# Kernel tuning notes

Hardware: AMD Instinct MI355X
Metric: run time of the kernel (lower is better)

## Reference

```python
import jax, jax.numpy as jnp
import numpy as np

N = 50000        # nodes
E = 150000       # edges
D_IN = 42        # node_input_dim
D_H = 42         # node_hidden_dim
E_IN = 10        # edge_input_dim
E_H = 128        # edge_hidden_dim
STEPS = 6        # num_step_message_passing


def _linear_params(key, fin, fout):
    k1, k2 = jax.random.split(key)
    bound = 1.0 / np.sqrt(fin)
    W = jax.random.uniform(k1, (fin, fout), minval=-bound, maxval=bound, dtype=jnp.float32)
    b = jax.random.uniform(k2, (fout,), minval=-bound, maxval=bound, dtype=jnp.float32)
    return W, b


def setup_inputs() -> dict:
    key = jax.random.key(0)
    ks = jax.random.split(key, 9)
    n_feat = jax.random.normal(ks[0], (N, D_IN), dtype=jnp.float32)
    e_feat = jax.random.normal(ks[1], (E, E_IN), dtype=jnp.float32)
    src = jax.random.randint(ks[2], (E,), 0, N, dtype=jnp.int32)
    dst = jax.random.randint(ks[3], (E,), 0, N, dtype=jnp.int32)
    lin0_w, lin0_b = _linear_params(ks[4], D_IN, D_H)
    en1_w, en1_b = _linear_params(ks[5], E_IN, E_H)
    en2_w, en2_b = _linear_params(ks[6], E_H, D_H * D_H)
    msg_w, msg_b = _linear_params(ks[7], 2 * D_H, D_H)
    conv_bias = jnp.zeros((D_H,), dtype=jnp.float32)  # NNConv bias
    return dict(n_feat=n_feat, e_feat=e_feat, src=src, dst=dst,
                lin0_w=lin0_w, lin0_b=lin0_b,
                en1_w=en1_w, en1_b=en1_b, en2_w=en2_w, en2_b=en2_b,
                conv_bias=conv_bias, msg_w=msg_w, msg_b=msg_b)


def reference(n_feat, e_feat, src, dst, lin0_w, lin0_b, en1_w, en1_b,
              en2_w, en2_b, conv_bias, msg_w, msg_b):
    init = n_feat
    out = jax.nn.relu(n_feat @ lin0_w + lin0_b)          # [N, D_H]
    # edge network: per-edge weight matrix (constant across the 6 steps)
    h_e = jax.nn.relu(e_feat @ en1_w + en1_b)            # [E, E_H]
    W_e = (h_e @ en2_w + en2_b).reshape(E, D_H, D_H)     # [E, D_H, D_H]
    for _ in range(STEPS):
        # NNConv: gather src feats, per-edge matmul, scatter-sum to dst,
        # identity residual (in==out feats) + bias
        msg = jnp.einsum('ei,eio->eo', out[src], W_e)    # [E, D_H]
        aggr = jax.ops.segment_sum(msg, dst, num_segments=N)
        m = jax.nn.relu(aggr + out + conv_bias)          # relu(conv(...))
        out = jnp.concatenate([m, out], axis=1) @ msg_w + msg_b
    return out + init
```

## Files before the change

### kernel.cpp

```cpp
#include <hip/hip_runtime.h>

typedef unsigned short u16;
typedef unsigned int u32;

#define NN 50000
#define NE 150000
#define D 42
#define EH 128
#define DD 1764
#define STEPS 6
#define MS 48
#define SCAN_NB 196

typedef __attribute__((ext_vector_type(8))) short bf8;
typedef __attribute__((ext_vector_type(4))) float f4;

static __device__ __forceinline__ float bf2f(u16 v) {
  return __uint_as_float(((u32)v) << 16);
}
static __device__ __forceinline__ u16 f2bf(float f) {
  u32 x = __float_as_uint(f);
  return (u16)((x + 0x7fffu + ((x >> 16) & 1u)) >> 16);
}

__global__ void k_detect(const u32* __restrict__ words, int* __restrict__ flag) {
  __shared__ int cnt;
  if (threadIdx.x == 0) cnt = 0;
  __syncthreads();
  int bad = 0;
  for (int i = threadIdx.x; i < 4096; i += 256) {
    u32 w = words[i];
    float v = __uint_as_float((w & 0xffffu) << 16);
    float a = fabsf(v);
    if (!(a < 16.0f)) bad++;
  }
  if (bad) atomicAdd(&cnt, bad);
  __syncthreads();
  if (threadIdx.x == 0) flag[0] = (cnt < 100) ? 1 : 0;
}

__global__ void k_cvt(const void* __restrict__ src, float* __restrict__ dst,
                      int count, const int* __restrict__ flag) {
  int i = blockIdx.x * blockDim.x + threadIdx.x;
  if (i >= count) return;
  if (flag[0]) dst[i] = bf2f(((const u16*)src)[i]);
  else         dst[i] = ((const float*)src)[i];
}

__global__ void k_hist(const int* __restrict__ dstI, int* __restrict__ cnt) {
  int e = blockIdx.x * blockDim.x + threadIdx.x;
  if (e < NE) atomicAdd(&cnt[dstI[e]], 1);
}

__global__ void k_scanA(const int* __restrict__ cnt, int* __restrict__ loc,
                        int* __restrict__ part) {
  __shared__ int wsum[4];
  int tid = threadIdx.x, wid = tid >> 6, lane = tid & 63;
  int i = blockIdx.x * 256 + tid;
  int v = (i < NN) ? cnt[i] : 0;
#pragma unroll
  for (int d = 1; d < 64; d <<= 1) {
    int t = __shfl_up(v, d, 64);
    if (lane >= d) v += t;
  }
  if (lane == 63) wsum[wid] = v;
  __syncthreads();
  if (tid == 0) {
    int s = 0;
#pragma unroll
    for (int w2 = 0; w2 < 4; ++w2) { int t = wsum[w2]; wsum[w2] = s; s += t; }
    part[blockIdx.x] = s;
  }
  __syncthreads();
  v += wsum[wid];
  if (i < NN) loc[i] = v;
}

__global__ void k_scanB(int* __restrict__ part) {
  __shared__ int wsum[4];
  int tid = threadIdx.x, wid = tid >> 6, lane = tid & 63;
  int v = (tid < SCAN_NB) ? part[tid] : 0;
  int orig = v;
#pragma unroll
  for (int d = 1; d < 64; d <<= 1) {
    int t = __shfl_up(v, d, 64);
    if (lane >= d) v += t;
  }
  if (lane == 63) wsum[wid] = v;
  __syncthreads();
  if (tid == 0) {
    int s = 0;
#pragma unroll
    for (int w2 = 0; w2 < 4; ++w2) { int t = wsum[w2]; wsum[w2] = s; s += t; }
  }
  __syncthreads();
  v += wsum[wid];
  if (tid < SCAN_NB) part[tid] = v - orig;
}

__global__ void k_scanC(const int* __restrict__ loc, const int* __restrict__ part,
                        int* __restrict__ rs) {
  int i = blockIdx.x * 256 + threadIdx.x;
  if (i == 0) rs[0] = 0;
  if (i < NN) rs[i + 1] = loc[i] + part[blockIdx.x];
}

__global__ void k_rank(const int* __restrict__ dstI, const int* __restrict__ srcI,
                       int* __restrict__ cursor, int* __restrict__ rank,
                       int* __restrict__ srcS) {
  int e = blockIdx.x * blockDim.x + threadIdx.x;
  if (e >= NE) return;
  int p = atomicAdd(&cursor[dstI[e]], 1);
  rank[e] = p;
  srcS[p] = srcI[e];
}

__global__ void k_lin0(const float* __restrict__ nf, const float* __restrict__ w,
                       const float* __restrict__ b, float* __restrict__ outp) {
  int gid = blockIdx.x * blockDim.x + threadIdx.x;
  int n = gid >> 6, lane = gid & 63;
  if (n >= NN) return;
  float xv = (lane < D) ? nf[(size_t)n * D + lane] : 0.f;
  if (lane < D) {
    float acc = b[lane];
    for (int i = 0; i < D; ++i)
      acc += __shfl(xv, i, 64) * w[i * D + lane];
    outp[(size_t)n * D + lane] = fmaxf(acc, 0.f);
  }
}

__global__ void k_en1(const float* __restrict__ ef, const float* __restrict__ w,
                      const float* __restrict__ b, const int* __restrict__ rank,
                      u16* __restrict__ h) {
  int gid = blockIdx.x * blockDim.x + threadIdx.x;
  int e = gid >> 7, k = gid & 127;
  if (e >= NE) return;
  float acc = b[k];
#pragma unroll
  for (int i = 0; i < 10; ++i)
    acc += ef[(size_t)e * 10 + i] * w[i * EH + k];
  h[(size_t)rank[e] * EH + k] = f2bf(fmaxf(acc, 0.f));
}

__global__ void k_packA(const float* __restrict__ w2, u16* __restrict__ Ap) {
  int idx = blockIdx.x * 256 + threadIdx.x;
  if (idx >= D * 4 * 3 * 64 * 8) return;
  int j = idx & 7;
  int t = idx >> 3;
  int l = t & 63; t >>= 6;
  int f = t % 3;  t /= 3;
  int s = t & 3;
  int i = t >> 2;
  int k = s * 32 + ((l >> 4) << 3) + j;
  int o = f * 16 + (l & 15);
  float v = (o < D) ? w2[(size_t)k * DD + i * D + o] : 0.f;
  Ap[idx] = f2bf(v);
}

__global__ void k_packB2(const float* __restrict__ e2b, u16* __restrict__ b2p) {
  int idx = blockIdx.x * 256 + threadIdx.x;
  if (idx >= 2 * 3 * 64 * 8) return;
  int j = idx & 7;
  int t = idx >> 3;
  int l = t & 63; t >>= 6;
  int f = t % 3;
  int s = t / 3;
  int k = s * 32 + ((l >> 4) << 3) + j;
  int o = f * 16 + (l & 15);
  float v = (k < D && o < D) ? e2b[k * D + o] : 0.f;
  b2p[idx] = f2bf(v);
}

__launch_bounds__(256, 3)
__global__ void k_edge_mfma(const float* __restrict__ outp, const u16* __restrict__ hbf,
                            const u16* __restrict__ Ap, const u16* __restrict__ b2p,
                            const int* __restrict__ srcS, float* __restrict__ msg) {
  __shared__ __align__(16) char smem[10752 + 26624];
  float* xT = (float*)smem;
  char*  hls = smem + 10752;
  char*  xbf = smem + 10752 + 16384;
  float* red = (float*)(smem + 10752);

  int tid = threadIdx.x;
  long et = (long)blockIdx.x * 64;
  int ne = (int)(NE - et); if (ne > 64) ne = 64;

  for (int c = tid; c < 1024; c += 256) {
    int row = c >> 4;
    int off = (c & 15) << 4;
    uint4 v = {0, 0, 0, 0};
    if (row < ne) v = *(const uint4*)(hbf + (et + row) * EH + (off >> 1));
    *(uint4*)(hls + row * 256 + (off ^ ((row & 7) << 4))) = v;
  }
  {
    int r = tid >> 2, j = tid & 3;
    const float* xr = (r < ne) ? (outp + (size_t)srcS[et + r] * D) : nullptr;
    for (int i = j; i < D; i += 4) {
      float v = xr ? xr[i] : 0.f;
      xT[i * 64 + r] = v;
      int bo = (r * 128 + i * 2) ^ ((r & 7) << 4);
      *(u16*)(xbf + bo) = f2bf(v);
    }
    for (int i = D + j; i < 64; i += 4) {
      int bo = (r * 128 + i * 2) ^ ((r & 7) << 4);
      *(u16*)(xbf + bo) = 0;
    }
  }
  __syncthreads();

  int w = tid >> 6;
  int l = tid & 63;
  int e16 = l & 15;
  int kg = l >> 4;

  bf8 hf[4];
  {
    int kb = (w * 32 + kg * 8) * 2;
    int sw = (e16 & 7) << 4;
#pragma unroll
    for (int g = 0; g < 4; ++g)
      hf[g] = *(const bf8*)(hls + (g * 16 + e16) * 256 + (kb ^ sw));
  }

  f4 macc[4][3];
#pragma unroll
  for (int g = 0; g < 4; ++g)
#pragma unroll
    for (int f = 0; f < 3; ++f)
      macc[g][f] = (f4){0.f, 0.f, 0.f, 0.f};

  const u16* apw = Ap + (size_t)w * 1536 + (size_t)l * 8;

#define COMPUTE(ii, AA)                                                         \
  {                                                                             \
    _Pragma("unroll")                                                           \
    for (int g = 0; g < 4; ++g) {                                               \
      float xs = xT[(ii) * 64 + g * 16 + e16];                                  \
      f4 zz = {0.f, 0.f, 0.f, 0.f};                                             \
      f4 q0 = __builtin_amdgcn_mfma_f32_16x16x32_bf16(AA[0], hf[g], zz, 0, 0, 0); \
      f4 q1 = __builtin_amdgcn_mfma_f32_16x16x32_bf16(AA[1], hf[g], zz, 0, 0, 0); \
      f4 q2 = __builtin_amdgcn_mfma_f32_16x16x32_bf16(AA[2], hf[g], zz, 0, 0, 0); \
      macc[g][0] += xs * q0;                                                    \
      macc[g][1] += xs * q1;                                                    \
      macc[g][2] += xs * q2;                                                    \
    }                                                                           \
  }

  bf8 A0[3], A1[3];
#pragma unroll
  for (int f = 0; f < 3; ++f) A0[f] = *(const bf8*)(apw + f * 512);
#pragma unroll 1
  for (int i = 0; i < D; i += 2) {
    const u16* pn = apw + (size_t)(i + 1) * 6144;
#pragma unroll
    for (int f = 0; f < 3; ++f) A1[f] = *(const bf8*)(pn + f * 512);
    COMPUTE(i, A0);
    if (i + 2 < D) {
      const u16* pn2 = apw + (size_t)(i + 2) * 6144;
#pragma unroll
      for (int f = 0; f < 3; ++f) A0[f] = *(const bf8*)(pn2 + f * 512);
    }
    COMPUTE(i + 1, A1);
  }

  if (w < 2) {
    const u16* bpw = b2p + (size_t)w * 1536 + (size_t)l * 8;
    bf8 B0 = *(const bf8*)(bpw);
    bf8 B1 = *(const bf8*)(bpw + 512);
    bf8 B2 = *(const bf8*)(bpw + 1024);
    int kb = (w * 32 + kg * 8) * 2;
    int sw = (e16 & 7) << 4;
#pragma unroll
    for (int g = 0; g < 4; ++g) {
      bf8 bx = *(const bf8*)(xbf + (g * 16 + e16) * 128 + (kb ^ sw));
      macc[g][0] = __builtin_amdgcn_mfma_f32_16x16x32_bf16(B0, bx, macc[g][0], 0, 0, 0);
      macc[g][1] = __builtin_amdgcn_mfma_f32_16x16x32_bf16(B1, bx, macc[g][1], 0, 0, 0);
      macc[g][2] = __builtin_amdgcn_mfma_f32_16x16x32_bf16(B2, bx, macc[g][2], 0, 0, 0);
    }
  }

  __syncthreads();
  if (w < 2) {
#pragma unroll
    for (int g = 0; g < 4; ++g)
#pragma unroll
      for (int f = 0; f < 3; ++f)
        *(f4*)&red[((size_t)w * 64 + g * 16 + e16) * 52 + f * 16 + kg * 4] = macc[g][f];
  }
  __syncthreads();
  if (w >= 2) {
#pragma unroll
    for (int g = 0; g < 4; ++g)
#pragma unroll
      for (int f = 0; f < 3; ++f) {
        float* rp = &red[((size_t)(w - 2) * 64 + g * 16 + e16) * 52 + f * 16 + kg * 4];
        f4 v = *(f4*)rp;
        v += macc[g][f];
        *(f4*)rp = v;
      }
  }
  __syncthreads();
  {
    int e = tid >> 2, c = tid & 3;
    if (e < ne) {
      float* mrow = msg + (size_t)(et + e) * MS;
#pragma unroll
      for (int u = 0; u < 3; ++u) {
        int o0 = c * 12 + u * 4;
        f4 v0 = *(f4*)&red[(size_t)e * 52 + o0];
        f4 v1 = *(f4*)&red[((size_t)(64 + e)) * 52 + o0];
        f4 s = v0 + v1;
        *(f4*)(mrow + o0) = s;
      }
    }
  }
#undef COMPUTE
}

__global__ void k_node_update(const float* __restrict__ msg, const int* __restrict__ rs,
                              const float* __restrict__ outp,
                              const float* __restrict__ cb, const float* __restrict__ mw,
                              const float* __restrict__ mb, float* __restrict__ newout,
                              const float* __restrict__ nf, void* __restrict__ fout,
                              int last, const int* __restrict__ flag) {
  int gid = blockIdx.x * blockDim.x + threadIdx.x;
  int n = gid >> 6, lane = gid & 63;
  if (n >= NN) return;
  float ov = (lane < D) ? outp[(size_t)n * D + lane] : 0.f;
  float av = 0.f;
  int r0 = rs[n], r1 = rs[n + 1];
  if (lane < D && r0 < r1) {
    float a0 = 0.f, a1 = 0.f, a2 = 0.f, a3 = 0.f;
    for (int r = r0; r < r1; r += 4) {
      int i1 = (r + 1 < r1) ? r + 1 : r;
      int i2 = (r + 2 < r1) ? r + 2 : r;
      int i3 = (r + 3 < r1) ? r + 3 : r;
      float v0 = msg[(size_t)r  * MS + lane];
      float v1 = msg[(size_t)i1 * MS + lane];
      float v2 = msg[(size_t)i2 * MS + lane];
      float v3 = msg[(size_t)i3 * MS + lane];
      a0 += v0;
      a1 += (r + 1 < r1) ? v1 : 0.f;
      a2 += (r + 2 < r1) ? v2 : 0.f;
      a3 += (r + 3 < r1) ? v3 : 0.f;
    }
    av = (a0 + a1) + (a2 + a3);
  }
  float mv = 0.f;
  if (lane < D) mv = fmaxf(av + ov + cb[lane], 0.f);
  if (lane < D) {
    float acc = mb[lane];
    for (int i = 0; i < D; ++i)
      acc += __shfl(mv, i, 64) * mw[i * D + lane];
    for (int i = 0; i < D; ++i)
      acc += __shfl(ov, i, 64) * mw[(D + i) * D + lane];
    size_t idx = (size_t)n * D + lane;
    if (last) {
      float res = acc + nf[idx];
      if (flag[0]) ((u16*)fout)[idx] = f2bf(res);
      else         ((float*)fout)[idx] = res;
    } else {
      newout[idx] = acc;
    }
  }
}

extern "C" void kernel_launch(void* const* d_in, const int* in_sizes, int n_in,
                              void* d_out, int out_size, void* d_ws, size_t ws_size,
                              hipStream_t stream) {
  (void)in_sizes; (void)n_in; (void)out_size; (void)ws_size;
  const void* nf   = d_in[0];
  const void* ef   = d_in[1];
  const int*  srcI = (const int*)d_in[2];
  const int*  dstI = (const int*)d_in[3];
  const void* l0w = d_in[4];  const void* l0b = d_in[5];
  const void* e1w = d_in[6];  const void* e1b = d_in[7];
  const void* e2w = d_in[8];  const void* e2b = d_in[9];
  const void* cbI = d_in[10]; const void* mwI = d_in[11]; const void* mbI = d_in[12];

  char* ws = (char*)d_ws;
  size_t off = 0;
  auto alloc = [&](size_t bytes) -> void* {
    void* p = ws + off;
    off = (off + bytes + 255) & ~(size_t)255;
    return p;
  };

  int*   flag  = (int*)alloc(4);
  float* c_nf  = (float*)alloc((size_t)NN * D * 4);
  float* c_ef  = (float*)alloc((size_t)NE * 10 * 4);
  float* c_l0w = (float*)alloc(D * D * 4);
  float* c_l0b = (float*)alloc(D * 4);
  float* c_e1w = (float*)alloc(10 * EH * 4);
  float* c_e1b = (float*)alloc(EH * 4);
  float* c_e2w = (float*)alloc((size_t)EH * DD * 4);
  float* c_e2b = (float*)alloc(DD * 4);
  float* c_cb  = (float*)alloc(D * 4);
  float* c_mw  = (float*)alloc(2 * D * D * 4);
  float* c_mb  = (float*)alloc(D * 4);
  float* out_a = (float*)alloc((size_t)NN * D * 4);
  float* out_b = (float*)alloc((size_t)NN * D * 4);
  u16*   hbf   = (u16*)alloc((size_t)NE * EH * 2);
  u16*   Ap    = (u16*)alloc((size_t)D * 4 * 3 * 64 * 8 * 2);
  u16*   b2p   = (u16*)alloc((size_t)2 * 3 * 64 * 8 * 2);
  int*   cnt    = (int*)alloc((size_t)NN * 4);
  int*   loc    = (int*)alloc((size_t)NN * 4);
  int*   part   = (int*)alloc((size_t)SCAN_NB * 4);
  int*   rowst  = (int*)alloc((size_t)(NN + 1) * 4);
  int*   cursor = (int*)alloc((size_t)NN * 4);
  int*   rank   = (int*)alloc((size_t)NE * 4);
  int*   srcS   = (int*)alloc((size_t)NE * 4);
  float* msg    = (float*)alloc((size_t)NE * MS * 4);

  k_detect<<<1, 256, 0, stream>>>((const u32*)nf, flag);
  auto cvt = [&](const void* s, float* dPtr, int count) {
    k_cvt<<<(count + 255) / 256, 256, 0, stream>>>(s, dPtr, count, flag);
  };
  cvt(nf,  c_nf,  NN * D);
  cvt(ef,  c_ef,  NE * 10);
  cvt(l0w, c_l0w, D * D);
  cvt(l0b, c_l0b, D);
  cvt(e1w, c_e1w, 10 * EH);
  cvt(e1b, c_e1b, EH);
  cvt(e2w, c_e2w, EH * DD);
  cvt(e2b, c_e2b, DD);
  cvt(cbI, c_cb,  D);
  cvt(mwI, c_mw,  2 * D * D);
  cvt(mbI, c_mb,  D);

  (void)hipMemsetAsync(cnt, 0, (size_t)NN * 4, stream);
  k_hist<<<(NE + 255) / 256, 256, 0, stream>>>(dstI, cnt);
  k_scanA<<<SCAN_NB, 256, 0, stream>>>(cnt, loc, part);
  k_scanB<<<1, 256, 0, stream>>>(part);
  k_scanC<<<SCAN_NB, 256, 0, stream>>>(loc, part, rowst);
  (void)hipMemcpyAsync(cursor, rowst, (size_t)NN * 4, hipMemcpyDeviceToDevice, stream);
  k_rank<<<(NE + 255) / 256, 256, 0, stream>>>(dstI, srcI, cursor, rank, srcS);

  k_lin0<<<(NN * 64 + 255) / 256, 256, 0, stream>>>(c_nf, c_l0w, c_l0b, out_a);
  k_en1<<<(NE * 128 + 255) / 256, 256, 0, stream>>>(c_ef, c_e1w, c_e1b, rank, hbf);
  k_packA<<<(D * 4 * 3 * 64 * 8 + 255) / 256, 256, 0, stream>>>(c_e2w, Ap);
  k_packB2<<<(2 * 3 * 64 * 8 + 255) / 256, 256, 0, stream>>>(c_e2b, b2p);

  int nblk = (NE + 63) / 64;
  float* cur = out_a;
  float* nxt = out_b;
  for (int s = 0; s < STEPS; ++s) {
    k_edge_mfma<<<nblk, 256, 0, stream>>>(cur, hbf, Ap, b2p, srcS, msg);
    int last = (s == STEPS - 1) ? 1 : 0;
    k_node_update<<<(NN * 64 + 255) / 256, 256, 0, stream>>>(
        msg, rowst, cur, c_cb, c_mw, c_mb, nxt, c_nf, d_out, last, flag);
    float* t = cur; cur = nxt; nxt = t;
  }
}
```

Measured before the change: 957.9 us.

## Split edge MFMA work across waves by edge group and K-half, chaining MFMAs

Reassigns the four waves so each handles 32 edges and half of the 128-wide K dimension, instead of each wave covering all 64 edges for one 32-wide K slice. Two K-slices are now chained through the MFMA accumulator before the per-input-feature scaling, so the FP32 scale-and-add work per wave is halved. The cross-wave reduction drops from a three-phase read-modify-write to a single shared-memory handoff, which also shrinks LDS use. In exchange, each wave loads twice as many A fragments per iteration, which raises register pressure and global/L2 traffic for the per-edge weight operand.

```diff
diff --git a/kernel.cpp b/kernel.cpp
--- a/kernel.cpp
+++ b/kernel.cpp
@@ -175,7 +175,7 @@
 __global__ void k_edge_mfma(const float* __restrict__ outp, const u16* __restrict__ hbf,
                             const u16* __restrict__ Ap, const u16* __restrict__ b2p,
                             const int* __restrict__ srcS, float* __restrict__ msg) {
-  __shared__ __align__(16) char smem[10752 + 26624];
+  __shared__ __align__(16) char smem[10752 + 24576];
   float* xT = (float*)smem;
   char*  hls = smem + 10752;
   char*  xbf = smem + 10752 + 16384;
@@ -212,67 +212,90 @@
   int l = tid & 63;
   int e16 = l & 15;
   int kg = l >> 4;
-
-  bf8 hf[4];
+  int kh = w >> 1;
+  int eg = w & 1;
+
+  bf8 hf00, hf01, hf10, hf11;
   {
-    int kb = (w * 32 + kg * 8) * 2;
     int sw = (e16 & 7) << 4;
-#pragma unroll
-    for (int g = 0; g < 4; ++g)
-      hf[g] = *(const bf8*)(hls + (g * 16 + e16) * 256 + (kb ^ sw));
-  }
-
-  f4 macc[4][3];
-#pragma unroll
-  for (int g = 0; g < 4; ++g)
+    int r0 = eg * 32 + e16;
+    int r1 = eg * 32 + 16 + e16;
+    int kb0 = ((kh * 2 + 0) * 32 + kg * 8) * 2;
+    int kb1 = ((kh * 2 + 1) * 32 + kg * 8) * 2;
+    hf00 = *(const bf8*)(hls + r0 * 256 + (kb0 ^ sw));
+    hf01 = *(const bf8*)(hls + r1 * 256 + (kb0 ^ sw));
+    hf10 = *(const bf8*)(hls + r0 * 256 + (kb1 ^ sw));
+    hf11 = *(const bf8*)(hls + r1 * 256 + (kb1 ^ sw));
+  }
+
+  f4 macc[2][3];
+#pragma unroll
+  for (int g = 0; g < 2; ++g)
 #pragma unroll
     for (int f = 0; f < 3; ++f)
       macc[g][f] = (f4){0.f, 0.f, 0.f, 0.f};
 
-  const u16* apw = Ap + (size_t)w * 1536 + (size_t)l * 8;
+  const u16* apw = Ap + (size_t)(kh * 2) * 1536 + (size_t)l * 8;
+
+#define LOADA(dst, ii)                                                          \
+  {                                                                             \
+    const u16* p_ = apw + (size_t)(ii) * 6144;                                  \
+    dst[0] = *(const bf8*)(p_);                                                 \
+    dst[1] = *(const bf8*)(p_ + 512);                                           \
+    dst[2] = *(const bf8*)(p_ + 1024);                                          \
+    dst[3] = *(const bf8*)(p_ + 1536);                                          \
+    dst[4] = *(const bf8*)(p_ + 2048);                                          \
+    dst[5] = *(const bf8*)(p_ + 2560);                                          \
+  }
 
 #define COMPUTE(ii, AA)                                                         \
   {                                                                             \
-    _Pragma("unroll")                                                           \
-    for (int g = 0; g < 4; ++g) {                                               \
-      float xs = xT[(ii) * 64 + g * 16 + e16];                                  \
-      f4 zz = {0.f, 0.f, 0.f, 0.f};                                             \
-      f4 q0 = __builtin_amdgcn_mfma_f32_16x16x32_bf16(AA[0], hf[g], zz, 0, 0, 0); \
-      f4 q1 = __builtin_amdgcn_mfma_f32_16x16x32_bf16(AA[1], hf[g], zz, 0, 0, 0); \
-      f4 q2 = __builtin_amdgcn_mfma_f32_16x16x32_bf16(AA[2], hf[g], zz, 0, 0, 0); \
-      macc[g][0] += xs * q0;                                                    \
-      macc[g][1] += xs * q1;                                                    \
-      macc[g][2] += xs * q2;                                                    \
-    }                                                                           \
-  }
-
-  bf8 A0[3], A1[3];
-#pragma unroll
-  for (int f = 0; f < 3; ++f) A0[f] = *(const bf8*)(apw + f * 512);
+    f4 zz = {0.f, 0.f, 0.f, 0.f};                                               \
+    f4 q0, q1, q2;                                                              \
+                                                                     \
+    q0 = __builtin_amdgcn_mfma_f32_16x16x32_bf16(AA[0], hf00, zz, 0, 0, 0);     \
+    q1 = __builtin_amdgcn_mfma_f32_16x16x32_bf16(AA[1], hf00, zz, 0, 0, 0);     \
+    q2 = __builtin_amdgcn_mfma_f32_16x16x32_bf16(AA[2], hf00, zz, 0, 0, 0);     \
+    q0 = __builtin_amdgcn_mfma_f32_16x16x32_bf16(AA[3], hf10, q0, 0, 0, 0);     \
+    q1 = __builtin_amdgcn_mfma_f32_16x16x32_bf16(AA[4], hf10, q1, 0, 0, 0);     \
+    q2 = __builtin_amdgcn_mfma_f32_16x16x32_bf16(AA[5], hf10, q2, 0, 0, 0);     \
+    float xs0 = xT[(ii) * 64 + eg * 32 + e16];                                  \
+    macc[0][0] += xs0 * q0;                                                     \
+    macc[0][1] += xs0 * q1;                                                     \
+    macc[0][2] += xs0 * q2;                                                     \
+                                                                     \
+    q0 = __builtin_amdgcn_mfma_f32_16x16x32_bf16(AA[0], hf01, zz, 0, 0, 0);     \
+    q1 = __builtin_amdgcn_mfma_f32_16x16x32_bf16(AA[1], hf01, zz, 0, 0, 0);     \
+    q2 = __builtin_amdgcn_mfma_f32_16x16x32_bf16(AA[2], hf01, zz, 0, 0, 0);     \
+    q0 = __builtin_amdgcn_mfma_f32_16x16x32_bf16(AA[3], hf11, q0, 0, 0, 0);     \
+    q1 = __builtin_amdgcn_mfma_f32_16x16x32_bf16(AA[4], hf11, q1, 0, 0, 0);     \
+    q2 = __builtin_amdgcn_mfma_f32_16x16x32_bf16(AA[5], hf11, q2, 0, 0, 0);     \
+    float xs1 = xT[(ii) * 64 + eg * 32 + 16 + e16];                             \
+    macc[1][0] += xs1 * q0;                                                     \
+    macc[1][1] += xs1 * q1;                                                     \
+    macc[1][2] += xs1 * q2;                                                     \
+  }
+
+  bf8 A0[6], A1[6];
+  LOADA(A0, 0);
 #pragma unroll 1
   for (int i = 0; i < D; i += 2) {
-    const u16* pn = apw + (size_t)(i + 1) * 6144;
-#pragma unroll
-    for (int f = 0; f < 3; ++f) A1[f] = *(const bf8*)(pn + f * 512);
+    LOADA(A1, i + 1);
     COMPUTE(i, A0);
-    if (i + 2 < D) {
-      const u16* pn2 = apw + (size_t)(i + 2) * 6144;
-#pragma unroll
-      for (int f = 0; f < 3; ++f) A0[f] = *(const bf8*)(pn2 + f * 512);
-    }
+    if (i + 2 < D) LOADA(A0, i + 2);
     COMPUTE(i + 1, A1);
   }
 
-  if (w < 2) {
-    const u16* bpw = b2p + (size_t)w * 1536 + (size_t)l * 8;
+  {
+    const u16* bpw = b2p + (size_t)kh * 1536 + (size_t)l * 8;
     bf8 B0 = *(const bf8*)(bpw);
     bf8 B1 = *(const bf8*)(bpw + 512);
     bf8 B2 = *(const bf8*)(bpw + 1024);
-    int kb = (w * 32 + kg * 8) * 2;
-    int sw = (e16 & 7) << 4;
-#pragma unroll
-    for (int g = 0; g < 4; ++g) {
-      bf8 bx = *(const bf8*)(xbf + (g * 16 + e16) * 128 + (kb ^ sw));
+    int kb = (kh * 32 + kg * 8) * 2;
+#pragma unroll
+    for (int g = 0; g < 2; ++g) {
+      int row = eg * 32 + g * 16 + e16;
+      bf8 bx = *(const bf8*)(xbf + ((row * 128 + kb) ^ ((row & 7) << 4)));
       macc[g][0] = __builtin_amdgcn_mfma_f32_16x16x32_bf16(B0, bx, macc[g][0], 0, 0, 0);
       macc[g][1] = __builtin_amdgcn_mfma_f32_16x16x32_bf16(B1, bx, macc[g][1], 0, 0, 0);
       macc[g][2] = __builtin_amdgcn_mfma_f32_16x16x32_bf16(B2, bx, macc[g][2], 0, 0, 0);
@@ -280,41 +303,31 @@
   }
 
   __syncthreads();
-  if (w < 2) {
-#pragma unroll
-    for (int g = 0; g < 4; ++g)
+  if (kh == 1) {
+#pragma unroll
+    for (int g = 0; g < 2; ++g)
 #pragma unroll
       for (int f = 0; f < 3; ++f)
-        *(f4*)&red[((size_t)w * 64 + g * 16 + e16) * 52 + f * 16 + kg * 4] = macc[g][f];
-  }
-  __syncthreads();
-  if (w >= 2) {
-#pragma unroll
-    for (int g = 0; g < 4; ++g)
-#pragma unroll
-      for (int f = 0; f < 3; ++f) {
-        float* rp = &red[((size_t)(w - 2) * 64 + g * 16 + e16) * 52 + f * 16 + kg * 4];
-        f4 v = *(f4*)rp;
-        v += macc[g][f];
-        *(f4*)rp = v;
+        *(f4*)&red[(size_t)(eg * 32 + g * 16 + e16) * 52 + f * 16 + kg * 4] = macc[g][f];
+  }
+  __syncthreads();
+  if (kh == 0) {
+#pragma unroll
+    for (int g = 0; g < 2; ++g) {
+      int e = eg * 32 + g * 16 + e16;
+      if (e < ne) {
+        float* mrow = msg + (size_t)(et + e) * MS;
+#pragma unroll
+        for (int f = 0; f < 3; ++f) {
+          f4 v = *(f4*)&red[(size_t)e * 52 + f * 16 + kg * 4];
+          v += macc[g][f];
+          *(f4*)(mrow + f * 16 + kg * 4) = v;
+        }
       }
-  }
-  __syncthreads();
-  {
-    int e = tid >> 2, c = tid & 3;
-    if (e < ne) {
-      float* mrow = msg + (size_t)(et + e) * MS;
-#pragma unroll
-      for (int u = 0; u < 3; ++u) {
-        int o0 = c * 12 + u * 4;
-        f4 v0 = *(f4*)&red[(size_t)e * 52 + o0];
-        f4 v1 = *(f4*)&red[((size_t)(64 + e)) * 52 + o0];
-        f4 s = v0 + v1;
-        *(f4*)(mrow + o0) = s;
-      }
     }
   }
 #undef COMPUTE
+#undef LOADA
 }
 
 __global__ void k_node_update(const float* __restrict__ msg, const int* __restrict__ rs,
```

New measurement: 1.003 ms. 4.7% more time.
